# Performance work log

Measured on AMD Instinct MI355X. Metric: run time of the kernel, lower is better.

## Reference

```python
import jax, jax.numpy as jnp
import numpy as np


def gcn_conv(x, src, dst, deg_inv_sqrt, W, b, n_nodes):
    # PyG GCNConv: linear transform first, then normalized aggregation (A_hat = D^-1/2 (A+I) D^-1/2)
    h = x @ W                                   # [N, out]
    norm = deg_inv_sqrt[src] * deg_inv_sqrt[dst]  # [E+N]
    msg = h[src] * norm[:, None]                # gather + scale
    out = jax.ops.segment_sum(msg, dst, num_segments=n_nodes)
    return out + b


def setup_inputs() -> dict:
    key = jax.random.key(0)
    ks = jax.random.split(key, 10)
    N, E, D_in, D_h = 50000, 640000, 128, 64
    x = jax.random.normal(ks[0], (N, D_in), dtype=jnp.float32)
    edge_index = jax.random.randint(ks[1], (2, E), 0, N, dtype=jnp.int64)

    def glorot(k, fan_in, fan_out):
        lim = jnp.sqrt(6.0 / (fan_in + fan_out)).astype(jnp.float32)
        return jax.random.uniform(k, (fan_in, fan_out), jnp.float32, -lim, lim)

    return {
        "x": x,
        "edge_index": edge_index,
        "W1": glorot(ks[2], D_in, D_h), "b1": jnp.zeros((D_h,), jnp.float32),
        "W2": glorot(ks[3], D_h, D_h),  "b2": jnp.zeros((D_h,), jnp.float32),
        "W3": glorot(ks[4], D_h, D_h),  "b3": jnp.zeros((D_h,), jnp.float32),
        "W4": glorot(ks[5], D_h, D_in), "b4": jnp.zeros((D_in,), jnp.float32),
    }


def reference(x, edge_index, W1, b1, W2, b2, W3, b3, W4, b4):
    n = x.shape[0]
    loops = jnp.arange(n, dtype=edge_index.dtype)
    src = jnp.concatenate([edge_index[0], loops])  # A + I self-loops
    dst = jnp.concatenate([edge_index[1], loops])
    deg = jax.ops.segment_sum(jnp.ones_like(dst, dtype=x.dtype), dst, num_segments=n)
    deg_inv_sqrt = jnp.where(deg > 0, jax.lax.rsqrt(deg), 0.0)

    h = jax.nn.relu(gcn_conv(x, src, dst, deg_inv_sqrt, W1, b1, n))
    # dropout is identity in eval mode
    z = jax.nn.relu(gcn_conv(h, src, dst, deg_inv_sqrt, W2, b2, n))
    x_hat = jax.nn.relu(gcn_conv(z, src, dst, deg_inv_sqrt, W3, b3, n))
    x_hat = gcn_conv(x_hat, src, dst, deg_inv_sqrt, W4, b4, n)
    return (x_hat, z)
```

## Files before the change

### kernel.cpp

```cpp
#include <hip/hip_runtime.h>
#include <hip/hip_bf16.h>


#define CPAD 16


__global__ __launch_bounds__(256) void init_all(int4* __restrict__ ell4, int nEll4,
                                                int* __restrict__ cursor, int N,
                                                unsigned* __restrict__ gAz,
                                                unsigned* __restrict__ gBz) {
    int i = blockIdx.x * 256 + threadIdx.x;
    if (i < nEll4) ell4[i] = make_int4(N, N, N, N);
    if (i < N) cursor[(size_t)i * CPAD] = 0;
    if (i < 32) { gAz[i] = 0u; gBz[i] = 0u; }
}

__global__ __launch_bounds__(256) void fill_ell(const int* __restrict__ src,
                                                const int* __restrict__ dst,
                                                int* __restrict__ cursor,
                                                int* __restrict__ ell, int E) {
    int e = blockIdx.x * 256 + threadIdx.x;
    if (e < E) {
        int d = dst[e];
        int slot = atomicAdd(&cursor[(size_t)d * CPAD], 1);
        if (slot < 64) ell[(size_t)d * 64 + slot] = src[e];
    }
}


__device__ __forceinline__ ushort r16(float f) {
    __hip_bfloat16 h = __float2bfloat16(f);
    return *reinterpret_cast<ushort*>(&h);
}
__device__ __forceinline__ float bf_lo(unsigned u) {
    return __builtin_bit_cast(float, u << 16);
}
__device__ __forceinline__ float bf_hi(unsigned u) {
    return __builtin_bit_cast(float, u & 0xFFFF0000u);
}

__device__ __forceinline__ void gather_pair_ell(const unsigned* __restrict__ G,
                                                const int* __restrict__ ell,
                                                int n0, int n1c,
                                                int lenA, int lenB, int lane,
                                                float& s0o, float& s1o,
                                                float& s2o, float& s3o) {
    int l32 = lane & 31;
    int idxA = ell[(size_t)n0 * 64 + l32];
    int idxB = ell[(size_t)n1c * 64 + l32];

    int grp     = lane >> 4;
    int p       = grp & 1;
    int nodeSel = grp >> 1;
    int f       = lane & 15;

    int cA = lenA < 32 ? lenA : 32;
    int cB = lenB < 32 ? lenB : 32;
    int cM = cA > cB ? cA : cB;
    int pM = (cM + 1) >> 1;

    float a0 = 0.f, a1 = 0.f, a2 = 0.f, a3 = 0.f;
    float b0 = 0.f, b1 = 0.f, b2 = 0.f, b3 = 0.f;

    for (int k = 0; k < pM; k += 8) {
        uint2 u[8];
#pragma unroll
        for (int i = 0; i < 8; ++i) {
            int e = p + 2 * (k + i);
            int sA = __shfl(idxA, e);
            int sB = __shfl(idxB, e);
            int s = nodeSel ? sB : sA;
            u[i] = *reinterpret_cast<const uint2*>(G + (unsigned)s * 32u + 2 * f);
        }
#pragma unroll
        for (int i = 0; i < 8; ++i) {
            if (i & 1) {
                b0 += bf_lo(u[i].x); b1 += bf_hi(u[i].x);
                b2 += bf_lo(u[i].y); b3 += bf_hi(u[i].y);
            } else {
                a0 += bf_lo(u[i].x); a1 += bf_hi(u[i].x);
                a2 += bf_lo(u[i].y); a3 += bf_hi(u[i].y);
            }
        }
    }
    int nOwn   = nodeSel ? n1c : n0;
    int lenOwn = nodeSel ? lenB : lenA;
    if (lenOwn > 64) lenOwn = 64;
    for (int e2 = 32 + p; e2 < lenOwn; e2 += 2) {
        int s = ell[(size_t)nOwn * 64 + e2];
        uint2 v = *reinterpret_cast<const uint2*>(G + (unsigned)s * 32u + 2 * f);
        a0 += bf_lo(v.x); a1 += bf_hi(v.x);
        a2 += bf_lo(v.y); a3 += bf_hi(v.y);
    }

    float r0 = a0 + b0, r1 = a1 + b1, r2 = a2 + b2, r3 = a3 + b3;
    r0 += __shfl_xor(r0, 16);
    r1 += __shfl_xor(r1, 16);
    r2 += __shfl_xor(r2, 16);
    r3 += __shfl_xor(r3, 16);
    s0o = r0; s1o = r1; s2o = r2; s3o = r3;
}

template <int K, int DOUT>
__global__ __launch_bounds__(256) void gemm_scale(const float* __restrict__ A,
                                                  const float* __restrict__ W,
                                                  const int* __restrict__ deg,
                                                  float* __restrict__ dis,
                                                  ushort* __restrict__ G16, int N) {
    constexpr int CG   = DOUT / 4;
    constexpr int RG   = 256 / CG;
    constexpr int ROWS = RG * 4;
    constexpr int LDA  = K + 4;

    __shared__ __align__(16) float a_lds[ROWS * LDA];
    __shared__ __align__(16) float w_lds[K * DOUT];

    int t    = threadIdx.x;
    int row0 = blockIdx.x * ROWS;

    constexpr int WF4 = K * DOUT / 4;
    for (int q = t; q < WF4; q += 256)
        reinterpret_cast<float4*>(w_lds)[q] =
            reinterpret_cast<const float4*>(W)[q];

    constexpr int AF4 = ROWS * K / 4;
    for (int q = t; q < AF4; q += 256) {
        int r  = q / (K / 4);
        int kc = q % (K / 4);
        float4 v = make_float4(0.f, 0.f, 0.f, 0.f);
        int gr = row0 + r;
        if (gr < N)
            v = reinterpret_cast<const float4*>(A + (size_t)gr * K)[kc];
        *reinterpret_cast<float4*>(&a_lds[r * LDA + kc * 4]) = v;
    }
    __syncthreads();

    int c0 = (t % CG) * 4;
    int r0 = (t / CG) * 4;

    float4 acc[4] = {};
#pragma unroll 1
    for (int k = 0; k < K; k += 4) {
        float4 w0 = *reinterpret_cast<const float4*>(&w_lds[(k + 0) * DOUT + c0]);
        float4 w1 = *reinterpret_cast<const float4*>(&w_lds[(k + 1) * DOUT + c0]);
        float4 w2 = *reinterpret_cast<const float4*>(&w_lds[(k + 2) * DOUT + c0]);
        float4 w3 = *reinterpret_cast<const float4*>(&w_lds[(k + 3) * DOUT + c0]);
#pragma unroll
        for (int j = 0; j < 4; ++j) {
            float4 a4 = *reinterpret_cast<const float4*>(&a_lds[(r0 + j) * LDA + k]);
            acc[j].x += a4.x * w0.x + a4.y * w1.x + a4.z * w2.x + a4.w * w3.x;
            acc[j].y += a4.x * w0.y + a4.y * w1.y + a4.z * w2.y + a4.w * w3.y;
            acc[j].z += a4.x * w0.z + a4.y * w1.z + a4.z * w2.z + a4.w * w3.z;
            acc[j].w += a4.x * w0.w + a4.y * w1.w + a4.z * w2.w + a4.w * w3.w;
        }
    }

#pragma unroll
    for (int j = 0; j < 4; ++j) {
        int gr = row0 + r0 + j;
        if (gr < N) {
            float dn = rsqrtf((float)(deg[(size_t)gr * CPAD] + 1));
            if (c0 == 0) dis[gr] = dn;
            float4 o = acc[j];
            ushort4 pk;
            pk.x = r16(o.x * dn); pk.y = r16(o.y * dn);
            pk.z = r16(o.z * dn); pk.w = r16(o.w * dn);
            *reinterpret_cast<ushort4*>(&G16[(size_t)gr * DOUT + c0]) = pk;
        }
    }
}

template <int K, int DOUT>
__global__ __launch_bounds__(256) void gemm_bias(const float* __restrict__ A,
                                                 const float* __restrict__ W,
                                                 const float* __restrict__ bias,
                                                 float* __restrict__ Out, int N) {
    constexpr int CG   = DOUT / 4;
    constexpr int RG   = 256 / CG;
    constexpr int ROWS = RG * 4;
    constexpr int LDA  = K + 4;

    __shared__ __align__(16) float a_lds[ROWS * LDA];
    __shared__ __align__(16) float w_lds[K * DOUT];

    int t    = threadIdx.x;
    int row0 = blockIdx.x * ROWS;

    constexpr int WF4 = K * DOUT / 4;
    for (int q = t; q < WF4; q += 256)
        reinterpret_cast<float4*>(w_lds)[q] =
            reinterpret_cast<const float4*>(W)[q];

    constexpr int AF4 = ROWS * K / 4;
    for (int q = t; q < AF4; q += 256) {
        int r  = q / (K / 4);
        int kc = q % (K / 4);
        float4 v = make_float4(0.f, 0.f, 0.f, 0.f);
        int gr = row0 + r;
        if (gr < N)
            v = reinterpret_cast<const float4*>(A + (size_t)gr * K)[kc];
        *reinterpret_cast<float4*>(&a_lds[r * LDA + kc * 4]) = v;
    }
    __syncthreads();

    int c0 = (t % CG) * 4;
    int r0 = (t / CG) * 4;

    float4 acc[4] = {};
#pragma unroll 1
    for (int k = 0; k < K; k += 4) {
        float4 w0 = *reinterpret_cast<const float4*>(&w_lds[(k + 0) * DOUT + c0]);
        float4 w1 = *reinterpret_cast<const float4*>(&w_lds[(k + 1) * DOUT + c0]);
        float4 w2 = *reinterpret_cast<const float4*>(&w_lds[(k + 2) * DOUT + c0]);
        float4 w3 = *reinterpret_cast<const float4*>(&w_lds[(k + 3) * DOUT + c0]);
#pragma unroll
        for (int j = 0; j < 4; ++j) {
            float4 a4 = *reinterpret_cast<const float4*>(&a_lds[(r0 + j) * LDA + k]);
            acc[j].x += a4.x * w0.x + a4.y * w1.x + a4.z * w2.x + a4.w * w3.x;
            acc[j].y += a4.x * w0.y + a4.y * w1.y + a4.z * w2.y + a4.w * w3.y;
            acc[j].z += a4.x * w0.z + a4.y * w1.z + a4.z * w2.z + a4.w * w3.z;
            acc[j].w += a4.x * w0.w + a4.y * w1.w + a4.z * w2.w + a4.w * w3.w;
        }
    }

    float4 b4v = *reinterpret_cast<const float4*>(&bias[c0]);
#pragma unroll
    for (int j = 0; j < 4; ++j) {
        int gr = row0 + r0 + j;
        if (gr < N) {
            float4 o = acc[j];
            o.x += b4v.x; o.y += b4v.y; o.z += b4v.z; o.w += b4v.w;
            reinterpret_cast<float4*>(Out + (size_t)gr * DOUT)[c0 / 4] = o;
        }
    }
}

template <bool WRITE_F32>
__global__ __launch_bounds__(256) void agg_gemm_pair(
    const unsigned* __restrict__ G,
    const int* __restrict__ deg,
    const int* __restrict__ ell,
    const float* __restrict__ dis,
    const float* __restrict__ bias,
    const float* __restrict__ Wn,
    unsigned* __restrict__ Gout,
    float* __restrict__ Zout,
    int N) {
    __shared__ __align__(16) float w_lds[64 * 64];
    __shared__ __align__(16) float a_buf[4][2][64];

    int t = threadIdx.x;
    for (int q = t; q < 64 * 64 / 4; q += 256)
        reinterpret_cast<float4*>(w_lds)[q] =
            reinterpret_cast<const float4*>(Wn)[q];
    __syncthreads();

    int wave = t >> 6, lane = t & 63;
    int h = lane >> 5, fl = lane & 31;
    int grp = lane >> 4, f = lane & 15;

    int n0 = (blockIdx.x * 4 + wave) * 2;
    if (n0 >= N) return;
    int n1 = n0 + 1;
    bool hasB = (n1 < N);
    int n1c = hasB ? n1 : n0;
    int nn = h ? n1c : n0;

    int lenA = deg[(size_t)n0 * CPAD];
    int lenB = hasB ? deg[(size_t)n1c * CPAD] : 0;

    float dn0 = dis[n0], dn1 = dis[n1c];
    uint2 us2 = *reinterpret_cast<const uint2*>(G + (size_t)nn * 32 + 2 * f);
    float4 b4 = reinterpret_cast<const float4*>(bias)[f];

    float s0, s1, s2, s3;
    gather_pair_ell(G, ell, n0, n1c, lenA, lenB, lane, s0, s1, s2, s3);

    float dn = h ? dn1 : dn0;
    float v0 = fmaxf(dn * (s0 + bf_lo(us2.x)) + b4.x, 0.f);
    float v1 = fmaxf(dn * (s1 + bf_hi(us2.x)) + b4.y, 0.f);
    float v2 = fmaxf(dn * (s2 + bf_lo(us2.y)) + b4.z, 0.f);
    float v3 = fmaxf(dn * (s3 + bf_hi(us2.y)) + b4.w, 0.f);

    if ((grp & 1) == 0)
        *reinterpret_cast<float4*>(&a_buf[wave][h][4 * f]) =
            make_float4(v0, v1, v2, v3);
    if (WRITE_F32 && (grp == 0 || (grp == 2 && hasB)))
        *reinterpret_cast<float4*>(Zout + (size_t)nn * 64 + 4 * f) =
            make_float4(v0, v1, v2, v3);

    __builtin_amdgcn_wave_barrier();

    float yA0 = 0.f, yA1 = 0.f, yA2 = 0.f, yA3 = 0.f;
    float yB0 = 0.f, yB1 = 0.f, yB2 = 0.f, yB3 = 0.f;
    for (int k = 0; k < 64; k += 4) {
        float4 a4 = *reinterpret_cast<const float4*>(&a_buf[wave][0][k]);
        float4 c4 = *reinterpret_cast<const float4*>(&a_buf[wave][1][k]);
        float w0 = w_lds[(k + 0) * 64 + lane];
        float w1 = w_lds[(k + 1) * 64 + lane];
        float w2 = w_lds[(k + 2) * 64 + lane];
        float w3 = w_lds[(k + 3) * 64 + lane];
        yA0 += a4.x * w0; yA1 += a4.y * w1; yA2 += a4.z * w2; yA3 += a4.w * w3;
        yB0 += c4.x * w0; yB1 += c4.y * w1; yB2 += c4.z * w2; yB3 += c4.w * w3;
    }
    float yA = (yA0 + yA1) + (yA2 + yA3);
    float yB = (yB0 + yB1) + (yB2 + yB3);

    float l0 = __shfl(yA, 2 * fl), h0 = __shfl(yA, 2 * fl + 1);
    float l1 = __shfl(yB, 2 * fl), h1 = __shfl(yB, 2 * fl + 1);
    float yl = h ? l1 : l0;
    float yh = h ? h1 : h0;
    if (h == 0 || hasB) {
        unsigned pk = (unsigned)r16(dn * yl) | ((unsigned)r16(dn * yh) << 16);
        Gout[(unsigned)nn * 32u + fl] = pk;
    }
}

__global__ __launch_bounds__(256) void aggregate_s3(
    const unsigned* __restrict__ G,
    const int* __restrict__ deg,
    const int* __restrict__ ell,
    const float* __restrict__ dis,
    const float* __restrict__ bias,
    unsigned* __restrict__ Out, int N) {
    int t = threadIdx.x;
    int wave = t >> 6, lane = t & 63;
    int h = lane >> 5;
    int grp = lane >> 4, f = lane & 15;

    int n0 = (blockIdx.x * 4 + wave) * 2;
    if (n0 >= N) return;
    int n1 = n0 + 1;
    bool hasB = (n1 < N);
    int n1c = hasB ? n1 : n0;
    int nn = h ? n1c : n0;

    int lenA = deg[(size_t)n0 * CPAD];
    int lenB = hasB ? deg[(size_t)n1c * CPAD] : 0;

    float dn0 = dis[n0], dn1 = dis[n1c];
    uint2 us2 = *reinterpret_cast<const uint2*>(G + (size_t)nn * 32 + 2 * f);
    float4 b4 = reinterpret_cast<const float4*>(bias)[f];

    float s0, s1, s2, s3;
    gather_pair_ell(G, ell, n0, n1c, lenA, lenB, lane, s0, s1, s2, s3);

    float dn = h ? dn1 : dn0;
    float o0 = fmaxf(dn * (s0 + bf_lo(us2.x)) + b4.x, 0.f);
    float o1 = fmaxf(dn * (s1 + bf_hi(us2.x)) + b4.y, 0.f);
    float o2 = fmaxf(dn * (s2 + bf_lo(us2.y)) + b4.z, 0.f);
    float o3 = fmaxf(dn * (s3 + bf_hi(us2.y)) + b4.w, 0.f);

    if (grp == 0 || (grp == 2 && hasB)) {
        uint2 pk2;
        pk2.x = (unsigned)r16(dn * o0) | ((unsigned)r16(dn * o1) << 16);
        pk2.y = (unsigned)r16(dn * o2) | ((unsigned)r16(dn * o3) << 16);
        *reinterpret_cast<uint2*>(Out + (size_t)nn * 32 + 2 * f) = pk2;
    }
}

__global__ __launch_bounds__(256) void aggregate_t(
    const unsigned* __restrict__ G,
    const int* __restrict__ deg,
    const int* __restrict__ ell,
    const float* __restrict__ dis,
    float* __restrict__ Out, int N) {
    int t = threadIdx.x;
    int wave = t >> 6, lane = t & 63;
    int h = lane >> 5;
    int grp = lane >> 4, f = lane & 15;

    int n0 = (blockIdx.x * 4 + wave) * 2;
    if (n0 >= N) return;
    int n1 = n0 + 1;
    bool hasB = (n1 < N);
    int n1c = hasB ? n1 : n0;
    int nn = h ? n1c : n0;

    int lenA = deg[(size_t)n0 * CPAD];
    int lenB = hasB ? deg[(size_t)n1c * CPAD] : 0;

    float dn0 = dis[n0], dn1 = dis[n1c];
    uint2 us2 = *reinterpret_cast<const uint2*>(G + (size_t)nn * 32 + 2 * f);

    float s0, s1, s2, s3;
    gather_pair_ell(G, ell, n0, n1c, lenA, lenB, lane, s0, s1, s2, s3);

    float dn = h ? dn1 : dn0;
    if (grp == 0 || (grp == 2 && hasB))
        *reinterpret_cast<float4*>(Out + (size_t)nn * 64 + 4 * f) =
            make_float4(dn * (s0 + bf_lo(us2.x)), dn * (s1 + bf_hi(us2.x)),
                        dn * (s2 + bf_lo(us2.y)), dn * (s3 + bf_hi(us2.y)));
}


extern "C" void kernel_launch(void* const* d_in, const int* in_sizes, int n_in,
                              void* d_out, int out_size, void* d_ws, size_t ws_size,
                              hipStream_t stream) {
    const float* x     = (const float*)d_in[0];
    const int*   edges = (const int*)d_in[1];
    const float* W1 = (const float*)d_in[2];
    const float* b1 = (const float*)d_in[3];
    const float* W2 = (const float*)d_in[4];
    const float* b2 = (const float*)d_in[5];
    const float* W3 = (const float*)d_in[6];
    const float* b3 = (const float*)d_in[7];
    const float* W4 = (const float*)d_in[8];
    const float* b4 = (const float*)d_in[9];

    const int DIN = 128, DH = 64;
    int N = in_sizes[0] / DIN;
    int E = in_sizes[1] / 2;

    const int* e_src = edges;
    const int* e_dst = edges + E;

    float* out   = (float*)d_out;
    float* x_hat = out;
    float* z     = out + (size_t)N * DIN;

    char*  ws  = (char*)d_ws;
    size_t woff = 0;
    auto carve = [&](size_t bytes) {
        void* p = ws + woff;
        woff = (woff + bytes + 255) & ~(size_t)255;
        return p;
    };
    float*    dis    = (float*)   carve((size_t)N * 4);
    int*      cursor = (int*)     carve((size_t)N * CPAD * 4);
    int*      ell    = (int*)     carve((size_t)N * 64 * 4);
    unsigned* gA     = (unsigned*)carve((size_t)(N + 1) * DH * 2);
    unsigned* gB     = (unsigned*)carve((size_t)(N + 1) * DH * 2);
    float*    tbuf   = (float*)   carve((size_t)N * DH * 4);
    (void)ws_size;

    int nb_e  = (E + 255) / 256;
    int nb_p  = (N + 7) / 8;
    int nEll4 = N * 16;

    init_all<<<(nEll4 + 255) / 256, 256, 0, stream>>>(
        (int4*)ell, nEll4, cursor, N,
        gA + (size_t)N * 32, gB + (size_t)N * 32);
    fill_ell<<<nb_e, 256, 0, stream>>>(e_src, e_dst, cursor, ell, E);

    gemm_scale<128, 64><<<(N + 63) / 64, 256, 0, stream>>>(
        x, W1, cursor, dis, (ushort*)gA, N);

    agg_gemm_pair<false><<<nb_p, 256, 0, stream>>>(
        gA, cursor, ell, dis, b1, W2, gB, nullptr, N);

    agg_gemm_pair<true><<<nb_p, 256, 0, stream>>>(
        gB, cursor, ell, dis, b2, W3, gA, z, N);

    aggregate_s3<<<nb_p, 256, 0, stream>>>(
        gA, cursor, ell, dis, b3, gB, N);

    aggregate_t<<<nb_p, 256, 0, stream>>>(
        gB, cursor, ell, dis, tbuf, N);
    gemm_bias<64, 128><<<(N + 31) / 32, 256, 0, stream>>>(tbuf, W4, b4, x_hat, N);
}
```

Measured before the change: 248.5 us.

## Split last two aggregation layers into feature halves for cache-resident gathers

The third layer's output is stored as two separate 32-feature bf16 planes. The last two aggregations now run per half, with a new gather routine that covers four edges per iteration over 8 feature lanes. Each pass gathers from a table half the size (about 3.2MB), which is meant to fit better in L2/MALL and cut random-gather misses. In exchange there are two more kernel launches and the edge lists are read twice, with fewer bytes fetched per gather.

```diff
diff --git a/kernel.cpp b/kernel.cpp
--- a/kernel.cpp
+++ b/kernel.cpp
@@ -7,12 +7,21 @@
 
 __global__ __launch_bounds__(256) void init_all(int4* __restrict__ ell4, int nEll4,
                                                 int* __restrict__ cursor, int N,
-                                                unsigned* __restrict__ gAz,
-                                                unsigned* __restrict__ gBz) {
+                                                unsigned* __restrict__ t1z,
+                                                unsigned* __restrict__ t2z,
+                                                unsigned* __restrict__ T3,
+                                                unsigned* __restrict__ T4) {
     int i = blockIdx.x * 256 + threadIdx.x;
     if (i < nEll4) ell4[i] = make_int4(N, N, N, N);
     if (i < N) cursor[(size_t)i * CPAD] = 0;
-    if (i < 32) { gAz[i] = 0u; gBz[i] = 0u; }
+    if (i < 32) { t1z[i] = 0u; t2z[i] = 0u; }
+    if (i < 16) {
+        size_t hs = (size_t)(N + 1) * 16;
+        T3[0 * hs + (size_t)N * 16 + i] = 0u;
+        T3[1 * hs + (size_t)N * 16 + i] = 0u;
+        T4[0 * hs + (size_t)N * 16 + i] = 0u;
+        T4[1 * hs + (size_t)N * 16 + i] = 0u;
+    }
 }
 
 __global__ __launch_bounds__(256) void fill_ell(const int* __restrict__ src,
@@ -99,6 +108,58 @@
     r2 += __shfl_xor(r2, 16);
     r3 += __shfl_xor(r3, 16);
     s0o = r0; s1o = r1; s2o = r2; s3o = r3;
+}
+
+__device__ __forceinline__ void gather_half(const unsigned* __restrict__ Gh,
+                                            const int* __restrict__ ell,
+                                            int n0, int n1c,
+                                            int lenA, int lenB, int lane,
+                                            float acc[4]) {
+    int l32 = lane & 31;
+    int idxA = ell[(size_t)n0 * 64 + l32];
+    int idxB = ell[(size_t)n1c * 64 + l32];
+
+    int j       = (lane >> 3) & 3;
+    int nodeSel = lane >> 5;
+    int f       = lane & 7;
+
+    int cA = lenA < 32 ? lenA : 32;
+    int cB = lenB < 32 ? lenB : 32;
+    int cM = cA > cB ? cA : cB;
+    int pM = (cM + 3) >> 2;
+
+    acc[0] = acc[1] = acc[2] = acc[3] = 0.f;
+
+    for (int k = 0; k < pM; k += 4) {
+        uint2 u[4];
+#pragma unroll
+        for (int i = 0; i < 4; ++i) {
+            int e = j + 4 * (k + i);
+            int sA = __shfl(idxA, e);
+            int sB = __shfl(idxB, e);
+            int s = nodeSel ? sB : sA;
+            u[i] = *reinterpret_cast<const uint2*>(Gh + (unsigned)s * 16u + 2 * f);
+        }
+#pragma unroll
+        for (int i = 0; i < 4; ++i) {
+            acc[0] += bf_lo(u[i].x); acc[1] += bf_hi(u[i].x);
+            acc[2] += bf_lo(u[i].y); acc[3] += bf_hi(u[i].y);
+        }
+    }
+    int nOwn   = nodeSel ? n1c : n0;
+    int lenOwn = nodeSel ? lenB : lenA;
+    if (lenOwn > 64) lenOwn = 64;
+    for (int e2 = 32 + j; e2 < lenOwn; e2 += 4) {
+        int s = ell[(size_t)nOwn * 64 + e2];
+        uint2 v = *reinterpret_cast<const uint2*>(Gh + (unsigned)s * 16u + 2 * f);
+        acc[0] += bf_lo(v.x); acc[1] += bf_hi(v.x);
+        acc[2] += bf_lo(v.y); acc[3] += bf_hi(v.y);
+    }
+#pragma unroll
+    for (int q = 0; q < 4; ++q) {
+        acc[q] += __shfl_xor(acc[q], 8);
+        acc[q] += __shfl_xor(acc[q], 16);
+    }
 }
 
 template <int K, int DOUT>
@@ -235,7 +296,7 @@
     }
 }
 
-template <bool WRITE_F32>
+template <bool WRITE_F32, bool SPLIT_OUT>
 __global__ __launch_bounds__(256) void agg_gemm_pair(
     const unsigned* __restrict__ G,
     const int* __restrict__ deg,
@@ -312,85 +373,93 @@
     float yh = h ? h1 : h0;
     if (h == 0 || hasB) {
         unsigned pk = (unsigned)r16(dn * yl) | ((unsigned)r16(dn * yh) << 16);
-        Gout[(unsigned)nn * 32u + fl] = pk;
-    }
-}
-
-__global__ __launch_bounds__(256) void aggregate_s3(
-    const unsigned* __restrict__ G,
+        if (SPLIT_OUT) {
+            int hf = fl >> 4, off = fl & 15;
+            Gout[(size_t)hf * (N + 1) * 16 + (size_t)nn * 16 + off] = pk;
+        } else {
+            Gout[(unsigned)nn * 32u + fl] = pk;
+        }
+    }
+}
+
+__global__ __launch_bounds__(256) void aggregate_s3_half(
+    const unsigned* __restrict__ T3,
     const int* __restrict__ deg,
     const int* __restrict__ ell,
     const float* __restrict__ dis,
     const float* __restrict__ bias,
-    unsigned* __restrict__ Out, int N) {
+    unsigned* __restrict__ T4,
+    int N, int hh) {
+    const unsigned* Gh = T3 + (size_t)hh * (N + 1) * 16;
+    unsigned* Oh = T4 + (size_t)hh * (N + 1) * 16;
+
     int t = threadIdx.x;
     int wave = t >> 6, lane = t & 63;
-    int h = lane >> 5;
-    int grp = lane >> 4, f = lane & 15;
+    int nodeSel = lane >> 5, j = (lane >> 3) & 3, f = lane & 7;
 
     int n0 = (blockIdx.x * 4 + wave) * 2;
     if (n0 >= N) return;
     int n1 = n0 + 1;
     bool hasB = (n1 < N);
     int n1c = hasB ? n1 : n0;
-    int nn = h ? n1c : n0;
+    int nn = nodeSel ? n1c : n0;
 
     int lenA = deg[(size_t)n0 * CPAD];
     int lenB = hasB ? deg[(size_t)n1c * CPAD] : 0;
 
-    float dn0 = dis[n0], dn1 = dis[n1c];
-    uint2 us2 = *reinterpret_cast<const uint2*>(G + (size_t)nn * 32 + 2 * f);
-    float4 b4 = reinterpret_cast<const float4*>(bias)[f];
-
-    float s0, s1, s2, s3;
-    gather_pair_ell(G, ell, n0, n1c, lenA, lenB, lane, s0, s1, s2, s3);
-
-    float dn = h ? dn1 : dn0;
-    float o0 = fmaxf(dn * (s0 + bf_lo(us2.x)) + b4.x, 0.f);
-    float o1 = fmaxf(dn * (s1 + bf_hi(us2.x)) + b4.y, 0.f);
-    float o2 = fmaxf(dn * (s2 + bf_lo(us2.y)) + b4.z, 0.f);
-    float o3 = fmaxf(dn * (s3 + bf_hi(us2.y)) + b4.w, 0.f);
-
-    if (grp == 0 || (grp == 2 && hasB)) {
-        uint2 pk2;
-        pk2.x = (unsigned)r16(dn * o0) | ((unsigned)r16(dn * o1) << 16);
-        pk2.y = (unsigned)r16(dn * o2) | ((unsigned)r16(dn * o3) << 16);
-        *reinterpret_cast<uint2*>(Out + (size_t)nn * 32 + 2 * f) = pk2;
-    }
-}
-
-__global__ __launch_bounds__(256) void aggregate_t(
-    const unsigned* __restrict__ G,
+    float dn = dis[nn];
+    uint2 us2 = *reinterpret_cast<const uint2*>(Gh + (size_t)nn * 16 + 2 * f);
+    float4 b4v = *reinterpret_cast<const float4*>(bias + hh * 32 + 4 * f);
+
+    float s[4];
+    gather_half(Gh, ell, n0, n1c, lenA, lenB, lane, s);
+
+    float o0 = fmaxf(dn * (s[0] + bf_lo(us2.x)) + b4v.x, 0.f);
+    float o1 = fmaxf(dn * (s[1] + bf_hi(us2.x)) + b4v.y, 0.f);
+    float o2 = fmaxf(dn * (s[2] + bf_lo(us2.y)) + b4v.z, 0.f);
+    float o3 = fmaxf(dn * (s[3] + bf_hi(us2.y)) + b4v.w, 0.f);
+
+    if (j == 0 && (nodeSel == 0 || hasB)) {
+        uint2 pk;
+        pk.x = (unsigned)r16(dn * o0) | ((unsigned)r16(dn * o1) << 16);
+        pk.y = (unsigned)r16(dn * o2) | ((unsigned)r16(dn * o3) << 16);
+        *reinterpret_cast<uint2*>(Oh + (size_t)nn * 16 + 2 * f) = pk;
+    }
+}
+
+__global__ __launch_bounds__(256) void aggregate_t_half(
+    const unsigned* __restrict__ T4,
     const int* __restrict__ deg,
     const int* __restrict__ ell,
     const float* __restrict__ dis,
-    float* __restrict__ Out, int N) {
+    float* __restrict__ Out,
+    int N, int hh) {
+    const unsigned* Gh = T4 + (size_t)hh * (N + 1) * 16;
+
     int t = threadIdx.x;
     int wave = t >> 6, lane = t & 63;
-    int h = lane >> 5;
-    int grp = lane >> 4, f = lane & 15;
+    int nodeSel = lane >> 5, j = (lane >> 3) & 3, f = lane & 7;
 
     int n0 = (blockIdx.x * 4 + wave) * 2;
     if (n0 >= N) return;
     int n1 = n0 + 1;
     bool hasB = (n1 < N);
     int n1c = hasB ? n1 : n0;
-    int nn = h ? n1c : n0;
+    int nn = nodeSel ? n1c : n0;
 
     int lenA = deg[(size_t)n0 * CPAD];
     int lenB = hasB ? deg[(size_t)n1c * CPAD] : 0;
 
-    float dn0 = dis[n0], dn1 = dis[n1c];
-    uint2 us2 = *reinterpret_cast<const uint2*>(G + (size_t)nn * 32 + 2 * f);
-
-    float s0, s1, s2, s3;
-    gather_pair_ell(G, ell, n0, n1c, lenA, lenB, lane, s0, s1, s2, s3);
-
-    float dn = h ? dn1 : dn0;
-    if (grp == 0 || (grp == 2 && hasB))
-        *reinterpret_cast<float4*>(Out + (size_t)nn * 64 + 4 * f) =
-            make_float4(dn * (s0 + bf_lo(us2.x)), dn * (s1 + bf_hi(us2.x)),
-                        dn * (s2 + bf_lo(us2.y)), dn * (s3 + bf_hi(us2.y)));
+    float dn = dis[nn];
+    uint2 us2 = *reinterpret_cast<const uint2*>(Gh + (size_t)nn * 16 + 2 * f);
+
+    float s[4];
+    gather_half(Gh, ell, n0, n1c, lenA, lenB, lane, s);
+
+    if (j == 0 && (nodeSel == 0 || hasB))
+        *reinterpret_cast<float4*>(Out + (size_t)nn * 64 + hh * 32 + 4 * f) =
+            make_float4(dn * (s[0] + bf_lo(us2.x)), dn * (s[1] + bf_hi(us2.x)),
+                        dn * (s[2] + bf_lo(us2.y)), dn * (s[3] + bf_hi(us2.y)));
 }
 
 
@@ -429,8 +498,10 @@
     float*    dis    = (float*)   carve((size_t)N * 4);
     int*      cursor = (int*)     carve((size_t)N * CPAD * 4);
     int*      ell    = (int*)     carve((size_t)N * 64 * 4);
-    unsigned* gA     = (unsigned*)carve((size_t)(N + 1) * DH * 2);
-    unsigned* gB     = (unsigned*)carve((size_t)(N + 1) * DH * 2);
+    unsigned* T1     = (unsigned*)carve((size_t)(N + 1) * DH * 2);
+    unsigned* T2     = (unsigned*)carve((size_t)(N + 1) * DH * 2);
+    unsigned* T3     = (unsigned*)carve((size_t)2 * (N + 1) * 16 * 4);
+    unsigned* T4     = (unsigned*)carve((size_t)2 * (N + 1) * 16 * 4);
     float*    tbuf   = (float*)   carve((size_t)N * DH * 4);
     (void)ws_size;
 
@@ -440,22 +511,26 @@
 
     init_all<<<(nEll4 + 255) / 256, 256, 0, stream>>>(
         (int4*)ell, nEll4, cursor, N,
-        gA + (size_t)N * 32, gB + (size_t)N * 32);
+        T1 + (size_t)N * 32, T2 + (size_t)N * 32, T3, T4);
     fill_ell<<<nb_e, 256, 0, stream>>>(e_src, e_dst, cursor, ell, E);
 
     gemm_scale<128, 64><<<(N + 63) / 64, 256, 0, stream>>>(
-        x, W1, cursor, dis, (ushort*)gA, N);
-
-    agg_gemm_pair<false><<<nb_p, 256, 0, stream>>>(
-        gA, cursor, ell, dis, b1, W2, gB, nullptr, N);
-
-    agg_gemm_pair<true><<<nb_p, 256, 0, stream>>>(
-        gB, cursor, ell, dis, b2, W3, gA, z, N);
-
-    aggregate_s3<<<nb_p, 256, 0, stream>>>(
-        gA, cursor, ell, dis, b3, gB, N);
-
-    aggregate_t<<<nb_p, 256, 0, stream>>>(
-        gB, cursor, ell, dis, tbuf, N);
+        x, W1, cursor, dis, (ushort*)T1, N);
+
+    agg_gemm_pair<false, false><<<nb_p, 256, 0, stream>>>(
+        T1, cursor, ell, dis, b1, W2, T2, nullptr, N);
+
+    agg_gemm_pair<true, true><<<nb_p, 256, 0, stream>>>(
+        T2, cursor, ell, dis, b2, W3, T3, z, N);
+
+    aggregate_s3_half<<<nb_p, 256, 0, stream>>>(
+        T3, cursor, ell, dis, b3, T4, N, 0);
+    aggregate_t_half<<<nb_p, 256, 0, stream>>>(
+        T4, cursor, ell, dis, tbuf, N, 0);
+    aggregate_s3_half<<<nb_p, 256, 0, stream>>>(
+        T3, cursor, ell, dis, b3, T4, N, 1);
+    aggregate_t_half<<<nb_p, 256, 0, stream>>>(
+        T4, cursor, ell, dis, tbuf, N, 1);
+
     gemm_bias<64, 128><<<(N + 31) / 32, 256, 0, stream>>>(tbuf, W4, b4, x_hat, N);
 }
```

Measured after the change: 265.8 us. 1.07x slower.
